# Optimization experiments

Measured on AMD Instinct MI355X. Metric: run time of the kernel, lower is better.

Reference implementation:

```python
import jax, jax.numpy as jnp
import numpy as np

B, S, E = 4, 2048, 1024

def setup_inputs() -> dict:
    key = jax.random.key(0)
    ks = jax.random.split(key, 4)
    scale = 1.0 / np.sqrt(E)
    x = jax.random.normal(ks[0], (B, S, E), dtype=jnp.float32)
    Wq = jax.random.normal(ks[1], (E, E), dtype=jnp.float32) * scale
    Wk = jax.random.normal(ks[2], (E, E), dtype=jnp.float32) * scale
    Wv = jax.random.normal(ks[3], (E, E), dtype=jnp.float32) * scale
    bq = jnp.zeros((E,), dtype=jnp.float32)
    bk = jnp.zeros((E,), dtype=jnp.float32)
    bv = jnp.zeros((E,), dtype=jnp.float32)
    # causal mask: 1 where attention allowed, 0 where blocked (masked_fill(mask==0, -inf))
    mask = jnp.tril(jnp.ones((S, S), dtype=jnp.int32))
    return {"x": x, "mask": mask, "Wq": Wq, "bq": bq, "Wk": Wk, "bk": bk, "Wv": Wv, "bv": bv}

def reference(x, mask, Wq, bq, Wk, bk, Wv, bv):
    # x: (B, S, E); mask: (S, S) int, 0 -> -inf. Matches torch nn.Linear: x @ W.T + b
    Q = jnp.einsum('bse,fe->bsf', x, Wq) + bq
    K = jnp.einsum('bse,fe->bsf', x, Wk) + bk
    V = jnp.einsum('bse,fe->bsf', x, Wv) + bv
    inv_sqrt_e = 1.0 / jnp.sqrt(jnp.asarray(x.shape[-1], dtype=x.dtype))
    scores = jnp.einsum('bqe,bke->bqk', Q, K) * inv_sqrt_e  # (B, S, S)
    scores = jnp.where(mask[None, :, :] == 0, jnp.asarray(-jnp.inf, scores.dtype), scores)
    attn = jax.nn.softmax(scores, axis=-1)
    out = jnp.einsum('bqk,bke->bqe', attn, V)  # (B, S, E)
    return out
```

## Files before the change

### kernel.cpp

```cpp
#include <hip/hip_runtime.h>

#define B_ 4
#define S_ 2048
#define E_ 1024

typedef __attribute__((ext_vector_type(8))) short short8;
typedef __attribute__((ext_vector_type(4))) float f32x4;

__device__ __forceinline__ unsigned short f2bu(float f) {
  unsigned u = __builtin_bit_cast(unsigned, f);
  u = (u + 0x7FFFu + ((u >> 16) & 1u)) >> 16;
  return (unsigned short)u;
}

__device__ __forceinline__ void gload_lds16(const void* g, void* l) {
  __builtin_amdgcn_global_load_lds(
      (const __attribute__((address_space(1))) void*)g,
      (__attribute__((address_space(3))) void*)l, 16, 0, 0);
}

__global__ __launch_bounds__(256) void cvt_f32_bf16(
    const float* __restrict__ in, unsigned short* __restrict__ out, int n) {
  int i = blockIdx.x * 256 + threadIdx.x;
  if (i * 4 >= n) return;
  float4 v = ((const float4*)in)[i];
  ushort4 o;
  o.x = f2bu(v.x); o.y = f2bu(v.y); o.z = f2bu(v.z); o.w = f2bu(v.w);
  ((ushort4*)out)[i] = o;
}

__global__ __launch_bounds__(256) void cvt_w3(
    const float* __restrict__ w0, const float* __restrict__ w1,
    const float* __restrict__ w2, unsigned short* __restrict__ out, int n) {
  int z = blockIdx.z;
  const float* in = (z == 0) ? w0 : (z == 1) ? w1 : w2;
  int i = blockIdx.x * 256 + threadIdx.x;
  if (i * 4 >= n) return;
  float4 v = ((const float4*)in)[i];
  ushort4 o;
  o.x = f2bu(v.x); o.y = f2bu(v.y); o.z = f2bu(v.z); o.w = f2bu(v.w);
  ((ushort4*)(out + (long)z * n))[i] = o;
}

__global__ __launch_bounds__(512, 2) void qkv8(
    const unsigned short* __restrict__ A, const unsigned short* __restrict__ W,
    const float* __restrict__ bq, const float* __restrict__ bk,
    const float* __restrict__ bv,
    unsigned short* __restrict__ Qo, unsigned short* __restrict__ Ko,
    unsigned short* __restrict__ Vt) {
  extern __shared__ char smem[];
  constexpr int NT = 16;
  int tid = threadIdx.x;
  int l = tid & 63, w = tid >> 6;
  int wm = w >> 2, wn = w & 3;
  int tm = blockIdx.y, tn = blockIdx.x;

  int scol = 8 * ((l & 7) ^ ((l >> 3) & 7));
  const unsigned short* Ag = A + (long)tm * 256 * 1024 + scol;
  const unsigned short* Bg = W + (long)tn * 128 * 1024 + scol;

#define STG_A(tt, h, q)                                                     \
  gload_lds16(Ag + ((long)(h) * 128 + (w * 2 + (q)) * 8 + (l >> 3)) * 1024  \
                  + (long)(tt) * 64,                                        \
              smem + ((tt) & 1) * 32768 + (h) * 16384 + (w * 2 + (q)) * 1024)
#define STG_B(tt, q)                                                        \
  gload_lds16(Bg + ((long)(w * 2 + (q)) * 8 + (l >> 3)) * 1024              \
                  + (long)(tt) * 64,                                        \
              smem + 65536 + ((tt) & 1) * 16384 + (w * 2 + (q)) * 1024)

  int xorc = (l & 7) << 4;
  int c0 = ((l >> 4) * 16) ^ xorc;
  int c1 = (64 + (l >> 4) * 16) ^ xorc;
  int arowbase = (wm * 128 + (l & 15)) * 128;
  int browbase = (wn * 32 + (l & 15)) * 128;

  f32x4 acc[8][2] = {};
  short8 a[4][2], b[2][2];

  STG_A(0, 0, 0); STG_A(0, 0, 1); STG_A(0, 1, 0); STG_A(0, 1, 1);
  STG_B(0, 0);    STG_B(0, 1);
  STG_A(1, 0, 0); STG_A(1, 0, 1); STG_A(1, 1, 0); STG_A(1, 1, 1);

#define PHASE_TAIL(h, j)                                                    \
  asm volatile("" ::: "memory");                                            \
  __builtin_amdgcn_s_barrier();                                             \
  asm volatile("s_waitcnt lgkmcnt(0)" ::: "memory");                        \
  __builtin_amdgcn_sched_barrier(0);                                        \
  __builtin_amdgcn_s_setprio(1);                                            \
  _Pragma("unroll")                                                         \
  for (int ii = 0; ii < 4; ii++) {                                          \
    acc[(h) * 4 + ii][j] = __builtin_amdgcn_mfma_f32_16x16x32_bf16(         \
        a[ii][0], b[j][0], acc[(h) * 4 + ii][j], 0, 0, 0);                  \
    acc[(h) * 4 + ii][j] = __builtin_amdgcn_mfma_f32_16x16x32_bf16(         \
        a[ii][1], b[j][1], acc[(h) * 4 + ii][j], 0, 0, 0);                  \
  }                                                                         \
  __builtin_amdgcn_s_setprio(0);                                            \
  __builtin_amdgcn_sched_barrier(0);                                        \
  asm volatile("" ::: "memory");                                            \
  __builtin_amdgcn_s_barrier();

  for (int t = 0; t < NT; ++t) {
    const char* Ad = smem + (t & 1) * 32768;
    const char* Bd = smem + 65536 + (t & 1) * 16384;
    if (t < NT - 1) asm volatile("s_waitcnt vmcnt(4)" ::: "memory");
    else            asm volatile("s_waitcnt vmcnt(0)" ::: "memory");
    __builtin_amdgcn_s_barrier();

#pragma unroll
    for (int ii = 0; ii < 4; ii++) {
      a[ii][0] = *(const short8*)(Ad + arowbase + ii * 2048 + c0);
      a[ii][1] = *(const short8*)(Ad + arowbase + ii * 2048 + c1);
    }
    b[0][0] = *(const short8*)(Bd + browbase + c0);
    b[0][1] = *(const short8*)(Bd + browbase + c1);
    if (t + 1 < NT) { STG_B(t + 1, 0); STG_B(t + 1, 1); }
    PHASE_TAIL(0, 0)

    b[1][0] = *(const short8*)(Bd + browbase + 2048 + c0);
    b[1][1] = *(const short8*)(Bd + browbase + 2048 + c1);
    PHASE_TAIL(0, 1)

#pragma unroll
    for (int ii = 0; ii < 4; ii++) {
      a[ii][0] = *(const short8*)(Ad + arowbase + 8192 + ii * 2048 + c0);
      a[ii][1] = *(const short8*)(Ad + arowbase + 8192 + ii * 2048 + c1);
    }
    PHASE_TAIL(1, 0)

    if (t + 2 < NT) { STG_A(t + 2, 0, 0); STG_A(t + 2, 0, 1);
                      STG_A(t + 2, 1, 0); STG_A(t + 2, 1, 1); }
    PHASE_TAIL(1, 1)
  }

  int rh = l >> 4, cl = l & 15;
  int colbase = tn * 128 + wn * 32 + cl;
  long rowbase = (long)tm * 256 + wm * 128 + rh * 4;
  int seg = tn >> 3;
  const float* bias = (seg == 0) ? bq : (seg == 1) ? bk : bv;
#pragma unroll
  for (int j = 0; j < 2; j++) {
    int c = colbase + j * 16;
    int cm = c & 1023;
    float bv_ = bias[cm];
#pragma unroll
    for (int i = 0; i < 8; i++) {
      long r0 = rowbase + i * 16;
      f32x4 v = acc[i][j];
      if (seg < 2) {
        unsigned short* Ch = seg ? Ko : Qo;
#pragma unroll
        for (int t4 = 0; t4 < 4; t4++)
          Ch[(r0 + t4) * (long)E_ + cm] = f2bu(v[t4] + bv_);
      } else {
        ushort4 pk;
        pk.x = f2bu(v[0] + bv_);
        pk.y = f2bu(v[1] + bv_);
        pk.z = f2bu(v[2] + bv_);
        pk.w = f2bu(v[3] + bv_);
        *(ushort4*)(Vt + (long)cm * (B_ * S_) + r0) = pk;
      }
    }
  }
#undef STG_A
#undef STG_B
#undef PHASE_TAIL
}

template<int MODE>
__global__ __launch_bounds__(256, 3) void gemm_bt(
    const unsigned short* __restrict__ A, long sAz, int lda,
    const unsigned short* __restrict__ B, long sBz, int ldb,
    void* __restrict__ C0, long sCz, int ldc, int K, float scale) {
  constexpr int BM = 128, BN = 128, BK = 64;
  __shared__ unsigned short lA[BM * BK];
  __shared__ unsigned short lB[BN * BK];
  int bm, bn;
  int bz = blockIdx.z;
  if constexpr (MODE == 1) {
    int t = blockIdx.x;
    bm = (int)((sqrtf(8.f * t + 1.f) - 1.f) * 0.5f);
    while ((bm + 1) * (bm + 2) / 2 <= t) bm++;
    while (bm * (bm + 1) / 2 > t) bm--;
    bn = t - bm * (bm + 1) / 2;
  } else {
    bm = blockIdx.y; bn = blockIdx.x;
  }
  const unsigned short* Ab = A + (long)bz * sAz + (long)bm * BM * lda;
  const unsigned short* Bb = B + (long)bz * sBz + (long)bn * BN * ldb;
  int Keff = (MODE == 2) ? min(K, (bm + 1) * BM) : K;

  int tid = threadIdx.x;
  int l = tid & 63, w = tid >> 6;
  int wm = w >> 1, wn = w & 1;

  int srow = l >> 3;
  int schunk = (l & 7) * 8;
  const unsigned short* ga[4];
  const unsigned short* gb[4];
  unsigned short* lad[4];
  unsigned short* lbd[4];
#pragma unroll
  for (int i = 0; i < 4; i++) {
    int seg = i * 4 + w;
    int row = seg * 8 + srow;
    ga[i] = Ab + (long)row * lda + schunk;
    gb[i] = Bb + (long)row * ldb + schunk;
    lad[i] = &lA[seg * 512];
    lbd[i] = &lB[seg * 512];
  }
  int aoff[4], boff[4];
#pragma unroll
  for (int i = 0; i < 4; i++) {
    aoff[i] = (wm * 64 + i * 16 + (l & 15)) * BK + (l >> 4) * 8;
    boff[i] = (wn * 64 + i * 16 + (l & 15)) * BK + (l >> 4) * 8;
  }

  f32x4 acc[4][4] = {};
  f32x4 accd[4] = {};
  short8 ones;
#pragma unroll
  for (int z = 0; z < 8; z++) ones[z] = (short)0x3F80;

  for (int k0 = 0; k0 < Keff; k0 += BK) {
    __syncthreads();
#pragma unroll
    for (int i = 0; i < 4; i++) {
      gload_lds16(ga[i], lad[i]);
      gload_lds16(gb[i], lbd[i]);
    }
#pragma unroll
    for (int i = 0; i < 4; i++) { ga[i] += BK; gb[i] += BK; }
    __syncthreads();
#pragma unroll
    for (int kk = 0; kk < 2; kk++) {
      short8 af[4], bf[4];
#pragma unroll
      for (int i = 0; i < 4; i++) af[i] = *(const short8*)&lA[aoff[i] + kk * 32];
#pragma unroll
      for (int j = 0; j < 4; j++) bf[j] = *(const short8*)&lB[boff[j] + kk * 32];
#pragma unroll
      for (int i = 0; i < 4; i++)
#pragma unroll
        for (int j = 0; j < 4; j++)
          acc[i][j] = __builtin_amdgcn_mfma_f32_16x16x32_bf16(af[i], bf[j], acc[i][j], 0, 0, 0);
      if constexpr (MODE == 2) {
#pragma unroll
        for (int i = 0; i < 4; i++)
          accd[i] = __builtin_amdgcn_mfma_f32_16x16x32_bf16(af[i], ones, accd[i], 0, 0, 0);
      }
    }
  }

  int rh = l >> 4, cl = l & 15;
  long rowbase = (long)bm * BM + wm * 64 + rh * 4;
  int colbase = bn * BN + wn * 64 + cl;

  if constexpr (MODE == 1) {
    unsigned short* Ph = (unsigned short*)C0 + (long)bz * sCz;
#pragma unroll
    for (int j = 0; j < 4; j++) {
      int c = colbase + j * 16;
#pragma unroll
      for (int i = 0; i < 4; i++) {
        int r0 = (int)rowbase + i * 16;
        f32x4 v = acc[i][j];
#pragma unroll
        for (int t = 0; t < 4; t++) {
          int r = r0 + t;
          float p = (c <= r) ? __expf(v[t] * scale) : 0.f;
          Ph[(long)r * ldc + c] = f2bu(p);
        }
      }
    }
  } else {
    float* Cf = (float*)C0 + (long)bz * sCz;
#pragma unroll
    for (int j = 0; j < 4; j++) {
      int c = colbase + j * 16;
#pragma unroll
      for (int i = 0; i < 4; i++) {
        long r0 = rowbase + i * 16;
        f32x4 v = acc[i][j];
        f32x4 d = accd[i];
#pragma unroll
        for (int t = 0; t < 4; t++)
          Cf[(r0 + t) * (long)ldc + c] = v[t] / d[t];
      }
    }
  }
}

extern "C" void kernel_launch(void* const* d_in, const int* in_sizes, int n_in,
                              void* d_out, int out_size, void* d_ws, size_t ws_size,
                              hipStream_t stream) {
  const float* x  = (const float*)d_in[0];
  const float* Wq = (const float*)d_in[2];
  const float* bq = (const float*)d_in[3];
  const float* Wk = (const float*)d_in[4];
  const float* bk = (const float*)d_in[5];
  const float* Wv = (const float*)d_in[6];
  const float* bv = (const float*)d_in[7];
  float* out = (float*)d_out;

  const long NX = (long)B_ * S_ * E_;
  const long NW = (long)E_ * E_;
  unsigned short* xb  = (unsigned short*)d_ws;
  unsigned short* wqb = xb + NX;
  unsigned short* Qb  = wqb + 3 * NW;
  unsigned short* Kb  = Qb + NX;
  unsigned short* Vtb = Kb + NX;
  unsigned short* Pb  = Vtb + NX;

  static int smem_set = 0;
  if (!smem_set) {
    hipFuncSetAttribute((const void*)qkv8,
                        hipFuncAttributeMaxDynamicSharedMemorySize, 98304);
    smem_set = 1;
  }

  cvt_f32_bf16<<<8192, 256, 0, stream>>>(x, xb, (int)NX);
  cvt_w3<<<dim3(1024, 1, 3), 256, 0, stream>>>(Wq, Wk, Wv, wqb, (int)NW);

  qkv8<<<dim3(24, 32), 512, 98304, stream>>>(
      xb, wqb, bq, bk, bv, Qb, Kb, Vtb);

  gemm_bt<1><<<dim3(136, 1, 4), 256, 0, stream>>>(
      Qb, (long)S_ * E_, E_, Kb, (long)S_ * E_, E_,
      Pb, (long)S_ * S_, S_, E_, 0.03125f);

  gemm_bt<2><<<dim3(8, 16, 4), 256, 0, stream>>>(
      Pb, (long)S_ * S_, S_,
      Vtb, (long)S_, B_ * S_,
      out, (long)S_ * E_, E_, S_, 1.f);
}
```

Before: 176.8 us.

## Enlarge QKV projection tile to 256x256 with swizzled block order

```diff
diff --git a/kernel.cpp b/kernel.cpp
--- a/kernel.cpp
+++ b/kernel.cpp
@@ -42,7 +42,7 @@
   ((ushort4*)(out + (long)z * n))[i] = o;
 }
 
-__global__ __launch_bounds__(512, 2) void qkv8(
+__global__ __launch_bounds__(512, 2) void qkv256(
     const unsigned short* __restrict__ A, const unsigned short* __restrict__ W,
     const float* __restrict__ bq, const float* __restrict__ bk,
     const float* __restrict__ bv,
@@ -53,99 +53,126 @@
   int tid = threadIdx.x;
   int l = tid & 63, w = tid >> 6;
   int wm = w >> 2, wn = w & 3;
-  int tm = blockIdx.y, tn = blockIdx.x;
+  int bid = blockIdx.y * 12 + blockIdx.x;
+  int swz = (bid & 7) * 48 + (bid >> 3);
+  int tm = swz / 12, tn = swz % 12;
 
   int scol = 8 * ((l & 7) ^ ((l >> 3) & 7));
   const unsigned short* Ag = A + (long)tm * 256 * 1024 + scol;
-  const unsigned short* Bg = W + (long)tn * 128 * 1024 + scol;
-
-#define STG_A(tt, h, q)                                                     \
-  gload_lds16(Ag + ((long)(h) * 128 + (w * 2 + (q)) * 8 + (l >> 3)) * 1024  \
-                  + (long)(tt) * 64,                                        \
+  const unsigned short* Bg = W + (long)tn * 256 * 1024 + scol;
+
+#define STG_A(tt, h, q)                                                  \
+  gload_lds16(Ag + (long)((h) * 128 + (w * 2 + (q)) * 8 + (l >> 3)) * 1024 \
+                  + (tt) * 64,                                           \
               smem + ((tt) & 1) * 32768 + (h) * 16384 + (w * 2 + (q)) * 1024)
-#define STG_B(tt, q)                                                        \
-  gload_lds16(Bg + ((long)(w * 2 + (q)) * 8 + (l >> 3)) * 1024              \
-                  + (long)(tt) * 64,                                        \
-              smem + 65536 + ((tt) & 1) * 16384 + (w * 2 + (q)) * 1024)
+#define STG_B(tt, h, q)                                                  \
+  gload_lds16(Bg + (long)((h) * 128 + (w * 2 + (q)) * 8 + (l >> 3)) * 1024 \
+                  + (tt) * 64,                                           \
+              smem + 65536 + ((tt) & 1) * 32768 + (h) * 16384 + (w * 2 + (q)) * 1024)
 
   int xorc = (l & 7) << 4;
   int c0 = ((l >> 4) * 16) ^ xorc;
   int c1 = (64 + (l >> 4) * 16) ^ xorc;
-  int arowbase = (wm * 128 + (l & 15)) * 128;
-  int browbase = (wn * 32 + (l & 15)) * 128;
-
-  f32x4 acc[8][2] = {};
-  short8 a[4][2], b[2][2];
-
-  STG_A(0, 0, 0); STG_A(0, 0, 1); STG_A(0, 1, 0); STG_A(0, 1, 1);
-  STG_B(0, 0);    STG_B(0, 1);
-  STG_A(1, 0, 0); STG_A(1, 0, 1); STG_A(1, 1, 0); STG_A(1, 1, 1);
-
-#define PHASE_TAIL(h, j)                                                    \
-  asm volatile("" ::: "memory");                                            \
-  __builtin_amdgcn_s_barrier();                                             \
-  asm volatile("s_waitcnt lgkmcnt(0)" ::: "memory");                        \
-  __builtin_amdgcn_sched_barrier(0);                                        \
-  __builtin_amdgcn_s_setprio(1);                                            \
-  _Pragma("unroll")                                                         \
-  for (int ii = 0; ii < 4; ii++) {                                          \
-    acc[(h) * 4 + ii][j] = __builtin_amdgcn_mfma_f32_16x16x32_bf16(         \
-        a[ii][0], b[j][0], acc[(h) * 4 + ii][j], 0, 0, 0);                  \
-    acc[(h) * 4 + ii][j] = __builtin_amdgcn_mfma_f32_16x16x32_bf16(         \
-        a[ii][1], b[j][1], acc[(h) * 4 + ii][j], 0, 0, 0);                  \
-  }                                                                         \
-  __builtin_amdgcn_s_setprio(0);                                            \
-  __builtin_amdgcn_sched_barrier(0);                                        \
-  asm volatile("" ::: "memory");                                            \
+  int arow = (wm * 128 + (l & 15)) * 128;
+  int brow = (wn * 64 + (l & 15)) * 128;
+
+  f32x4 acc[8][4] = {};
+  short8 a[4][2], b[2][2][2];
+
+  STG_A(0, 0, 0); STG_A(0, 0, 1); STG_B(0, 0, 0); STG_B(0, 0, 1);
+  STG_B(0, 1, 0); STG_B(0, 1, 1); STG_A(0, 1, 0); STG_A(0, 1, 1);
+  STG_A(1, 0, 0); STG_A(1, 0, 1); STG_B(1, 0, 0); STG_B(1, 0, 1);
+  STG_B(1, 1, 0); STG_B(1, 1, 1); STG_A(1, 1, 0); STG_A(1, 1, 1);
+  asm volatile("s_waitcnt vmcnt(8)" ::: "memory");
   __builtin_amdgcn_s_barrier();
+
+#define BAR_IN                                             \
+  asm volatile("" ::: "memory");                           \
+  __builtin_amdgcn_s_barrier();                            \
+  asm volatile("s_waitcnt lgkmcnt(0)" ::: "memory");       \
+  __builtin_amdgcn_sched_barrier(0);                       \
+  __builtin_amdgcn_s_setprio(1);
+#define BAR_OUT                                            \
+  __builtin_amdgcn_s_setprio(0);                           \
+  __builtin_amdgcn_sched_barrier(0);                       \
+  asm volatile("" ::: "memory");                           \
+  __builtin_amdgcn_s_barrier();
+#define MFMA_Q(MH, NH)                                                    \
+  _Pragma("unroll")                                                       \
+  for (int mf = 0; mf < 4; mf++) {                                        \
+    _Pragma("unroll")                                                     \
+    for (int nf = 0; nf < 2; nf++) {                                      \
+      acc[(MH) * 4 + mf][(NH) * 2 + nf] =                                 \
+          __builtin_amdgcn_mfma_f32_16x16x32_bf16(                        \
+              a[mf][0], b[NH][nf][0], acc[(MH) * 4 + mf][(NH) * 2 + nf],  \
+              0, 0, 0);                                                   \
+      acc[(MH) * 4 + mf][(NH) * 2 + nf] =                                 \
+          __builtin_amdgcn_mfma_f32_16x16x32_bf16(                        \
+              a[mf][1], b[NH][nf][1], acc[(MH) * 4 + mf][(NH) * 2 + nf],  \
+              0, 0, 0);                                                   \
+    }                                                                     \
+  }
 
   for (int t = 0; t < NT; ++t) {
     const char* Ad = smem + (t & 1) * 32768;
-    const char* Bd = smem + 65536 + (t & 1) * 16384;
-    if (t < NT - 1) asm volatile("s_waitcnt vmcnt(4)" ::: "memory");
-    else            asm volatile("s_waitcnt vmcnt(0)" ::: "memory");
-    __builtin_amdgcn_s_barrier();
-
-#pragma unroll
-    for (int ii = 0; ii < 4; ii++) {
-      a[ii][0] = *(const short8*)(Ad + arowbase + ii * 2048 + c0);
-      a[ii][1] = *(const short8*)(Ad + arowbase + ii * 2048 + c1);
-    }
-    b[0][0] = *(const short8*)(Bd + browbase + c0);
-    b[0][1] = *(const short8*)(Bd + browbase + c1);
-    if (t + 1 < NT) { STG_B(t + 1, 0); STG_B(t + 1, 1); }
-    PHASE_TAIL(0, 0)
-
-    b[1][0] = *(const short8*)(Bd + browbase + 2048 + c0);
-    b[1][1] = *(const short8*)(Bd + browbase + 2048 + c1);
-    PHASE_TAIL(0, 1)
-
-#pragma unroll
-    for (int ii = 0; ii < 4; ii++) {
-      a[ii][0] = *(const short8*)(Ad + arowbase + 8192 + ii * 2048 + c0);
-      a[ii][1] = *(const short8*)(Ad + arowbase + 8192 + ii * 2048 + c1);
-    }
-    PHASE_TAIL(1, 0)
+    const char* Bd = smem + 65536 + (t & 1) * 32768;
+
+#pragma unroll
+    for (int mf = 0; mf < 4; mf++) {
+      a[mf][0] = *(const short8*)(Ad + arow + mf * 2048 + c0);
+      a[mf][1] = *(const short8*)(Ad + arow + mf * 2048 + c1);
+    }
+#pragma unroll
+    for (int nf = 0; nf < 2; nf++) {
+      b[0][nf][0] = *(const short8*)(Bd + brow + nf * 2048 + c0);
+      b[0][nf][1] = *(const short8*)(Bd + brow + nf * 2048 + c1);
+    }
+    BAR_IN
+    MFMA_Q(0, 0)
+    BAR_OUT
+
+#pragma unroll
+    for (int nf = 0; nf < 2; nf++) {
+      b[1][nf][0] = *(const short8*)(Bd + brow + 4096 + nf * 2048 + c0);
+      b[1][nf][1] = *(const short8*)(Bd + brow + 4096 + nf * 2048 + c1);
+    }
+    BAR_IN
+    MFMA_Q(0, 1)
+    BAR_OUT
+
+#pragma unroll
+    for (int mf = 0; mf < 4; mf++) {
+      a[mf][0] = *(const short8*)(Ad + arow + 8192 + mf * 2048 + c0);
+      a[mf][1] = *(const short8*)(Ad + arow + 8192 + mf * 2048 + c1);
+    }
+    if (t + 2 < NT) { STG_B(t + 2, 0, 0); STG_B(t + 2, 0, 1);
+                      STG_B(t + 2, 1, 0); STG_B(t + 2, 1, 1); }
+    BAR_IN
+    MFMA_Q(1, 0)
+    BAR_OUT
 
     if (t + 2 < NT) { STG_A(t + 2, 0, 0); STG_A(t + 2, 0, 1);
                       STG_A(t + 2, 1, 0); STG_A(t + 2, 1, 1); }
-    PHASE_TAIL(1, 1)
+    if (t < NT - 2)       asm volatile("s_waitcnt vmcnt(8)" ::: "memory");
+    else if (t == NT - 2) asm volatile("s_waitcnt vmcnt(0)" ::: "memory");
+    BAR_IN
+    MFMA_Q(1, 1)
+    BAR_OUT
   }
 
   int rh = l >> 4, cl = l & 15;
-  int colbase = tn * 128 + wn * 32 + cl;
+  int seg = tn >> 2;
+  const float* bias = (seg == 0) ? bq : (seg == 1) ? bk : bv;
   long rowbase = (long)tm * 256 + wm * 128 + rh * 4;
-  int seg = tn >> 3;
-  const float* bias = (seg == 0) ? bq : (seg == 1) ? bk : bv;
-#pragma unroll
-  for (int j = 0; j < 2; j++) {
-    int c = colbase + j * 16;
-    int cm = c & 1023;
+  int cmbase = (tn & 3) * 256 + wn * 64 + cl;
+#pragma unroll
+  for (int nf = 0; nf < 4; nf++) {
+    int cm = cmbase + nf * 16;
     float bv_ = bias[cm];
 #pragma unroll
-    for (int i = 0; i < 8; i++) {
-      long r0 = rowbase + i * 16;
-      f32x4 v = acc[i][j];
+    for (int mf = 0; mf < 8; mf++) {
+      long r0 = rowbase + mf * 16;
+      f32x4 v = acc[mf][nf];
       if (seg < 2) {
         unsigned short* Ch = seg ? Ko : Qo;
 #pragma unroll
@@ -163,7 +190,9 @@
   }
 #undef STG_A
 #undef STG_B
-#undef PHASE_TAIL
+#undef BAR_IN
+#undef BAR_OUT
+#undef MFMA_Q
 }
 
 template<int MODE>
@@ -313,15 +342,15 @@
 
   static int smem_set = 0;
   if (!smem_set) {
-    hipFuncSetAttribute((const void*)qkv8,
-                        hipFuncAttributeMaxDynamicSharedMemorySize, 98304);
+    hipFuncSetAttribute((const void*)qkv256,
+                        hipFuncAttributeMaxDynamicSharedMemorySize, 131072);
     smem_set = 1;
   }
 
   cvt_f32_bf16<<<8192, 256, 0, stream>>>(x, xb, (int)NX);
   cvt_w3<<<dim3(1024, 1, 3), 256, 0, stream>>>(Wq, Wk, Wv, wqb, (int)NW);
 
-  qkv8<<<dim3(24, 32), 512, 98304, stream>>>(
+  qkv256<<<dim3(12, 32), 512, 131072, stream>>>(
       xb, wqb, bq, bk, bv, Qb, Kb, Vtb);
 
   gemm_bt<1><<<dim3(136, 1, 4), 256, 0, stream>>>(
```

New measurement: 183.6 us. 1.04x slower.
